# Kernel tuning notes

Measured on AMD Instinct MI355X. Metric: run time of the kernel, lower is better.

The kernel has to match this reference:

```python
import jax, jax.numpy as jnp
import numpy as np
from jax import lax

K = 7            # pool_size / PSROI_BINS
C_OUT = 10       # output channels per bin (features has K*K*C_OUT channels)
FEAT_STRIDE = 16
LAMDA = 0.1
SAMPLES = 2      # bilinear sample points per bin side
H = W = 200
C_IN = K * K * C_OUT  # 490
N_ROIS = 512


def setup_inputs() -> dict:
    key = jax.random.key(0)
    k1, k2, k3, k4 = jax.random.split(key, 4)
    features = jax.random.normal(k1, (1, H, W, C_IN), jnp.float32)
    conv_w = jax.random.truncated_normal(k2, -2.0, 2.0, (3, 3, C_IN, 2 * K * K), jnp.float32) * 0.01
    img = H * FEAT_STRIDE  # image-space extent
    cxy = jax.random.uniform(k3, (N_ROIS, 2), minval=0.0, maxval=img - 1.0)
    wh = jax.random.uniform(k4, (N_ROIS, 2), minval=64.0, maxval=640.0)
    x1 = jnp.clip(cxy[:, 0] - wh[:, 0] * 0.5, 0.0, img - 2.0)
    y1 = jnp.clip(cxy[:, 1] - wh[:, 1] * 0.5, 0.0, img - 2.0)
    x2 = jnp.clip(x1 + wh[:, 0], x1 + 1.0, img - 1.0)
    y2 = jnp.clip(y1 + wh[:, 1], y1 + 1.0, img - 1.0)
    rois = jnp.stack([jnp.zeros(N_ROIS), x1, y1, x2, y2], axis=-1)  # [N,5]
    return {"features": features, "rois": rois, "conv_w": conv_w}


def _bilinear(feat, y, x):
    """feat [H,W,C]; y,x arbitrary equal shapes -> [..., C]."""
    Hf, Wf = feat.shape[0], feat.shape[1]
    y = jnp.clip(y, 0.0, Hf - 1.0)
    x = jnp.clip(x, 0.0, Wf - 1.0)
    y0 = jnp.floor(y)
    x0 = jnp.floor(x)
    y0i = y0.astype(jnp.int32)
    x0i = x0.astype(jnp.int32)
    y1i = jnp.minimum(y0i + 1, Hf - 1)
    x1i = jnp.minimum(x0i + 1, Wf - 1)
    wy = (y - y0)[..., None]
    wx = (x - x0)[..., None]
    v00 = feat[y0i, x0i]
    v01 = feat[y0i, x1i]
    v10 = feat[y1i, x0i]
    v11 = feat[y1i, x1i]
    return (v00 * (1 - wy) * (1 - wx) + v01 * (1 - wy) * wx
            + v10 * wy * (1 - wx) + v11 * wy * wx)


def _ps_roi(feat, box, cpg, offsets):
    """Position-sensitive RoI avg pooling with optional per-bin offsets.
    feat [H,W,K*K*cpg]; box (x1,y1,x2,y2) image coords; offsets [K,K,2] (dx,dy)
    in image coords or None. Returns [K,K,cpg]."""
    x1, y1, x2, y2 = box
    fx1 = x1 / FEAT_STRIDE
    fy1 = y1 / FEAT_STRIDE
    bw = (x2 - x1 + 1.0) / FEAT_STRIDE / K
    bh = (y2 - y1 + 1.0) / FEAT_STRIDE / K
    idx = jnp.arange(K, dtype=feat.dtype)
    s = (jnp.arange(SAMPLES, dtype=feat.dtype) + 0.5) / SAMPLES
    sx = fx1 + (idx[:, None] + s[None, :]) * bw  # [K(j), S]
    sy = fy1 + (idx[:, None] + s[None, :]) * bh  # [K(i), S]
    gx = jnp.broadcast_to(sx[None, :, None, :], (K, K, SAMPLES, SAMPLES))
    gy = jnp.broadcast_to(sy[:, None, :, None], (K, K, SAMPLES, SAMPLES))
    if offsets is not None:
        off = offsets / FEAT_STRIDE  # image -> feature coords
        gx = gx + off[..., 0][:, :, None, None]
        gy = gy + off[..., 1][:, :, None, None]
    vals = _bilinear(feat, gy, gx)                     # [K,K,S,S,K*K*cpg]
    vals = vals.reshape(K, K, SAMPLES, SAMPLES, K * K, cpg)
    bin_idx = (jnp.arange(K)[:, None] * K + jnp.arange(K)[None, :])  # [K,K]
    sel = jnp.take_along_axis(
        vals, bin_idx[:, :, None, None, None, None], axis=4)[..., 0, :]
    return sel.mean(axis=(2, 3))  # [K,K,cpg]


def reference(features, rois, conv_w):
    # 3x3 same conv producing 2*K*K offset channels (no bias)
    offset_map = lax.conv_general_dilated(
        features, conv_w, (1, 1), 'SAME',
        dimension_numbers=('NHWC', 'HWIO', 'NHWC'))[0]  # [H,W,2*K*K]
    feat0 = features[0]  # [H,W,K*K*C_OUT]

    def one_roi(roi):
        x1, y1, x2, y2 = roi[1], roi[2], roi[3], roi[4]
        rw = x2 - x1 + 1.0
        rh = y2 - y1 + 1.0
        box = (x1, y1, x2, y2)
        # stage 1: pool the offset map position-sensitively -> [K,K,2]
        off = _ps_roi(offset_map, box, 2, None).reshape(-1, 2)
        off = jnp.stack((off[:, 0] * rw * LAMDA,
                         off[:, 1] * rh * LAMDA), axis=-1).reshape(K, K, 2)
        # stage 2: deformable PS-RoI pooling of the features -> [K,K,C_OUT]
        return _ps_roi(feat0, box, C_OUT, off)

    return jax.vmap(one_roi)(rois)  # [N, K, K, C_OUT]
```

## Files before the change

### kernel.cpp

```cpp
#include <hip/hip_runtime.h>
#include <hip/hip_bf16.h>

#define Hh   200
#define Ww   200
#define CIN  490
#define OCN  98
#define KK   7
#define COUT 10
#define NROIS 512
#define PIX  8

#define PH   202
#define PW   202
#define PC   512
#define NPIX (Hh * Ww)
#define KCN  16
#define NF   7
#define NUNITS 144
#define NGRAN  36

typedef __attribute__((ext_vector_type(8))) short short8;
typedef __attribute__((ext_vector_type(4))) float float4v;

__global__ __launch_bounds__(256) void pack_feat_kernel(
    const float* __restrict__ feat, __hip_bfloat16* __restrict__ pf)
{
    int tid = blockIdx.x * 256 + threadIdx.x;
    if (tid >= PH * PW * (PC / 8)) return;
    int c8  = (tid & 63) * 8;
    int pix = tid >> 6;
    int py = pix / PW, px = pix % PW;
    __hip_bfloat16* dst = pf + (size_t)pix * PC + c8;
    bool interior = (py >= 1 && py <= Hh && px >= 1 && px <= Ww);

    __hip_bfloat16 v[8];
    if (interior && c8 + 8 <= CIN) {
        const float* s = feat + ((size_t)(py - 1) * Ww + (px - 1)) * CIN + c8;
#pragma unroll
        for (int q = 0; q < 4; ++q) {
            float2 f2 = *reinterpret_cast<const float2*>(s + q * 2);
            v[q * 2]     = __float2bfloat16(f2.x);
            v[q * 2 + 1] = __float2bfloat16(f2.y);
        }
    } else {
        const float* s = interior ? feat + ((size_t)(py - 1) * Ww + (px - 1)) * CIN : nullptr;
#pragma unroll
        for (int j = 0; j < 8; ++j) {
            float val = (interior && (c8 + j) < CIN) ? s[c8 + j] : 0.f;
            v[j] = __float2bfloat16(val);
        }
    }
    *reinterpret_cast<short8*>(dst) = *reinterpret_cast<short8*>(v);
}

__global__ __launch_bounds__(256) void pack_w_kernel(
    const float* __restrict__ w, __hip_bfloat16* __restrict__ bp)
{
    int idx = blockIdx.x * 256 + threadIdx.x;
    if (idx >= NUNITS * NF * 64 * 8) return;
    int j = idx & 7;
    int l = (idx >> 3) & 63;
    int f = (idx >> 9) % NF;
    int u = idx / (NF * 512);
    int tap = u / KCN, kc = u % KCN;
    int k = kc * 32 + ((l >> 4) * 8) + j;
    int n = f * 16 + (l & 15);
    float val = (k < CIN && n < OCN) ? w[((size_t)tap * CIN + k) * OCN + n] : 0.f;
    bp[idx] = __float2bfloat16(val);
}

__global__ __launch_bounds__(640) void conv_mfma_kernel(
    const short* __restrict__ pf,
    const short* __restrict__ bp,
    float* __restrict__ om)
{
    __shared__ short bsm[8 * 3584];

    int l = threadIdx.x & 63;
    int w = threadIdx.x >> 6;
    int m0 = blockIdx.x * 160 + w * 16;

    int row = m0 + (l & 15);
    int y = row / Ww, x = row % Ww;
    const short* abase = pf + ((size_t)(y * PW + x) * PC) + ((l >> 4) * 8);

    float4v acc[NF];
#pragma unroll
    for (int f = 0; f < NF; ++f) acc[f] = (float4v){0.f, 0.f, 0.f, 0.f};

    auto aAddr = [&](int u) -> const short* {
        int tap = u >> 4, kc = u & 15;
        int ky = tap / 3, kx = tap % 3;
        return abase + (ky * PW + kx) * PC + kc * 32;
    };

    {
#pragma unroll
        for (int s = 0; s < 3; ++s) {
            int i = w + s * 10;
            if (i < 28) {
                int u = i / 7, f = i % 7;
                short8 v = *reinterpret_cast<const short8*>(
                    bp + ((size_t)(u * NF + f)) * 512 + l * 8);
                *reinterpret_cast<short8*>(&bsm[(u & 7) * 3584 + f * 512 + l * 8]) = v;
            }
        }
    }
    short8 a0 = *reinterpret_cast<const short8*>(aAddr(0));
    short8 a1 = *reinterpret_cast<const short8*>(aAddr(1));
    short8 a2 = *reinterpret_cast<const short8*>(aAddr(2));
    short8 a3 = *reinterpret_cast<const short8*>(aAddr(3));
    __syncthreads();

    for (int g = 0; g < NGRAN; ++g) {
        bool more = (g < NGRAN - 1);
        int u0n = (g + 1) * 4;

        short8 st0, st1, st2;
        int off0 = -1, off1 = -1, off2 = -1;
        if (more) {
            {
                int i = w;
                int uu = u0n + i / 7, f = i % 7;
                st0 = *reinterpret_cast<const short8*>(
                    bp + ((size_t)(uu * NF + f)) * 512 + l * 8);
                off0 = (uu & 7) * 3584 + f * 512 + l * 8;
            }
            {
                int i = w + 10;
                int uu = u0n + i / 7, f = i % 7;
                st1 = *reinterpret_cast<const short8*>(
                    bp + ((size_t)(uu * NF + f)) * 512 + l * 8);
                off1 = (uu & 7) * 3584 + f * 512 + l * 8;
            }
            if (w + 20 < 28) {
                int i = w + 20;
                int uu = u0n + i / 7, f = i % 7;
                st2 = *reinterpret_cast<const short8*>(
                    bp + ((size_t)(uu * NF + f)) * 512 + l * 8);
                off2 = (uu & 7) * 3584 + f * 512 + l * 8;
            }
        }
        short8 n0, n1, n2, n3;
        if (more) {
            n0 = *reinterpret_cast<const short8*>(aAddr(u0n + 0));
            n1 = *reinterpret_cast<const short8*>(aAddr(u0n + 1));
            n2 = *reinterpret_cast<const short8*>(aAddr(u0n + 2));
            n3 = *reinterpret_cast<const short8*>(aAddr(u0n + 3));
        }

        int u0 = g * 4;
#define COMPUTE_UNIT(J, AREG)                                                   \
        {                                                                       \
            int sbase = ((u0 + J) & 7) * 3584 + l * 8;                          \
            _Pragma("unroll")                                                   \
            for (int f = 0; f < NF; ++f) {                                      \
                short8 b = *reinterpret_cast<short8*>(&bsm[sbase + f * 512]);   \
                acc[f] = __builtin_amdgcn_mfma_f32_16x16x32_bf16(               \
                    AREG, b, acc[f], 0, 0, 0);                                  \
            }                                                                   \
        }
        COMPUTE_UNIT(0, a0)
        COMPUTE_UNIT(1, a1)
        COMPUTE_UNIT(2, a2)
        COMPUTE_UNIT(3, a3)
#undef COMPUTE_UNIT

        if (off0 >= 0) *reinterpret_cast<short8*>(&bsm[off0]) = st0;
        if (off1 >= 0) *reinterpret_cast<short8*>(&bsm[off1]) = st1;
        if (off2 >= 0) *reinterpret_cast<short8*>(&bsm[off2]) = st2;
        if (more) { a0 = n0; a1 = n1; a2 = n2; a3 = n3; }
        __syncthreads();
    }

    int n = l & 15;
    int rbase = m0 + ((l >> 4) * 4);
#pragma unroll
    for (int f = 0; f < NF; ++f) {
        int col = f * 16 + n;
        if (col < OCN) {
#pragma unroll
            for (int j = 0; j < 4; ++j)
                om[(size_t)(rbase + j) * OCN + col] = acc[f][j];
        }
    }
}

__global__ __launch_bounds__(256) void conv3x3_kernel(
    const float* __restrict__ feat, const float* __restrict__ w,
    const float* __restrict__ zero, float* __restrict__ om)
{
    int idx = blockIdx.x * blockDim.x + threadIdx.x;
    if (idx >= Hh * (Ww / PIX) * OCN) return;
    int oc = idx % OCN;
    int g  = idx / OCN;
    int x0 = (g % (Ww / PIX)) * PIX;
    int y  = g / (Ww / PIX);

    float acc[PIX];
#pragma unroll
    for (int p = 0; p < PIX; ++p) acc[p] = 0.f;

    for (int ky = 0; ky < 3; ++ky) {
        int yy = y + ky - 1;
        if (yy < 0 || yy >= Hh) continue;
        const float* frow = feat + (size_t)yy * Ww * CIN;
        for (int kx = 0; kx < 3; ++kx) {
            const float* wp = w + ((ky * 3 + kx) * CIN) * OCN + oc;
            const float* fp[PIX];
#pragma unroll
            for (int p = 0; p < PIX; ++p) {
                int xx = x0 + p + kx - 1;
                fp[p] = (xx >= 0 && xx < Ww) ? (frow + (size_t)xx * CIN) : zero;
            }
            for (int ic = 0; ic < CIN; ic += 2) {
                float w0 = wp[ic * OCN];
                float w1 = wp[(ic + 1) * OCN];
#pragma unroll
                for (int p = 0; p < PIX; ++p) {
                    float2 f = *reinterpret_cast<const float2*>(fp[p] + ic);
                    acc[p] = fmaf(f.x, w0, acc[p]);
                    acc[p] = fmaf(f.y, w1, acc[p]);
                }
            }
        }
    }
    float* orow = om + ((size_t)y * Ww + x0) * OCN + oc;
#pragma unroll
    for (int p = 0; p < PIX; ++p) orow[p * OCN] = acc[p];
}

__device__ __forceinline__ void bilin_setup(float y, float x,
    int& i00, int& i01, int& i10, int& i11,
    float& w00, float& w01, float& w10, float& w11)
{
    y = fminf(fmaxf(y, 0.f), 199.f);
    x = fminf(fmaxf(x, 0.f), 199.f);
    float y0f = floorf(y), x0f = floorf(x);
    int y0 = (int)y0f, x0i = (int)x0f;
    int y1 = min(y0 + 1, 199), x1 = min(x0i + 1, 199);
    float wy = y - y0f, wx = x - x0f;
    i00 = y0 * Ww + x0i;  i01 = y0 * Ww + x1;
    i10 = y1 * Ww + x0i;  i11 = y1 * Ww + x1;
    w00 = (1.f - wy) * (1.f - wx);
    w01 = (1.f - wy) * wx;
    w10 = wy * (1.f - wx);
    w11 = wy * wx;
}

__global__ __launch_bounds__(256) void psroi_kernel(
    const float* __restrict__ feat, const float* __restrict__ rois,
    const float* __restrict__ om, float* __restrict__ out)
{
    int n = blockIdx.x;
    int t = threadIdx.x;

    float x1 = rois[n * 5 + 1], y1 = rois[n * 5 + 2];
    float x2 = rois[n * 5 + 3], y2 = rois[n * 5 + 4];
    float rw = x2 - x1 + 1.0f, rh = y2 - y1 + 1.0f;
    float fx1 = x1 * 0.0625f, fy1 = y1 * 0.0625f;
    float bw = (rw * 0.0625f) / 7.0f;
    float bh = (rh * 0.0625f) / 7.0f;

    __shared__ float offs[49][2];

    if (t < 49) {
        int bi = t / 7, bj = t % 7;
        float ax = 0.f, ay = 0.f;
#pragma unroll
        for (int ss = 0; ss < 4; ++ss) {
            float sj = ((float)(ss & 1) + 0.5f) * 0.5f;
            float si = ((float)(ss >> 1) + 0.5f) * 0.5f;
            float gx = fx1 + ((float)bj + sj) * bw;
            float gy = fy1 + ((float)bi + si) * bh;
            int i00, i01, i10, i11; float w00, w01, w10, w11;
            bilin_setup(gy, gx, i00, i01, i10, i11, w00, w01, w10, w11);
            int c0 = t * 2;
            const float* p00 = om + (size_t)i00 * OCN + c0;
            const float* p01 = om + (size_t)i01 * OCN + c0;
            const float* p10 = om + (size_t)i10 * OCN + c0;
            const float* p11 = om + (size_t)i11 * OCN + c0;
            ax += w00 * p00[0] + w01 * p01[0] + w10 * p10[0] + w11 * p11[0];
            ay += w00 * p00[1] + w01 * p01[1] + w10 * p10[1] + w11 * p11[1];
        }
        offs[t][0] = ax * 0.25f * rw * 0.1f * 0.0625f;
        offs[t][1] = ay * 0.25f * rh * 0.1f * 0.0625f;
    }
    __syncthreads();

    for (int o = t; o < KK * KK * COUT; o += blockDim.x) {
        int bin = o / COUT, c = o % COUT;
        int bi = bin / 7, bj = bin % 7;
        float dx = offs[bin][0], dy = offs[bin][1];
        int ch = bin * COUT + c;
        float acc = 0.f;
#pragma unroll
        for (int ss = 0; ss < 4; ++ss) {
            float sj = ((float)(ss & 1) + 0.5f) * 0.5f;
            float si = ((float)(ss >> 1) + 0.5f) * 0.5f;
            float gx = fx1 + ((float)bj + sj) * bw + dx;
            float gy = fy1 + ((float)bi + si) * bh + dy;
            int i00, i01, i10, i11; float w00, w01, w10, w11;
            bilin_setup(gy, gx, i00, i01, i10, i11, w00, w01, w10, w11);
            acc += w00 * feat[(size_t)i00 * CIN + ch]
                 + w01 * feat[(size_t)i01 * CIN + ch]
                 + w10 * feat[(size_t)i10 * CIN + ch]
                 + w11 * feat[(size_t)i11 * CIN + ch];
        }
        out[(size_t)n * (KK * KK * COUT) + o] = acc * 0.25f;
    }
}

extern "C" void kernel_launch(void* const* d_in, const int* in_sizes, int n_in,
                              void* d_out, int out_size, void* d_ws, size_t ws_size,
                              hipStream_t stream) {
    const float* feat = (const float*)d_in[0];
    const float* rois = (const float*)d_in[1];
    const float* w    = (const float*)d_in[2];
    float* out = (float*)d_out;

    const size_t OM_BYTES = (size_t)NPIX * OCN * 4;
    const size_t BP_BYTES = (size_t)NUNITS * NF * 64 * 8 * 2;
    const size_t PF_BYTES = (size_t)PH * PW * PC * 2;
    const size_t NEEDED = OM_BYTES + BP_BYTES + PF_BYTES;

    if (ws_size >= NEEDED) {
        float* om = (float*)d_ws;
        __hip_bfloat16* bp = (__hip_bfloat16*)((char*)d_ws + OM_BYTES);
        __hip_bfloat16* pf = (__hip_bfloat16*)((char*)d_ws + OM_BYTES + BP_BYTES);

        int wThreads = NUNITS * NF * 64 * 8;
        pack_w_kernel<<<(wThreads + 255) / 256, 256, 0, stream>>>(w, bp);
        int fThreads = PH * PW * (PC / 8);
        pack_feat_kernel<<<(fThreads + 255) / 256, 256, 0, stream>>>(feat, pf);
        conv_mfma_kernel<<<250, 640, 0, stream>>>(
            (const short*)pf, (const short*)bp, om);
        psroi_kernel<<<NROIS, 256, 0, stream>>>(feat, rois, om, out);
    } else {
        float* zero = (float*)d_ws;
        float* om   = (float*)d_ws + 1024;
        hipMemsetAsync(d_ws, 0, 4096, stream);
        int convThreads = Hh * (Ww / PIX) * OCN;
        conv3x3_kernel<<<(convThreads + 255) / 256, 256, 0, stream>>>(feat, w, zero, om);
        psroi_kernel<<<NROIS, 256, 0, stream>>>(feat, rois, om, out);
    }
}
```

Before: 96.75 us.

## Register-block two M tiles per wave and remap blocks for XCD locality

Each wave now computes two 16-row M tiles sharing every B fragment read from LDS, with blocks of 5 waves instead of 10, so each LDS B load feeds two MFMAs. Block indices are also remapped so consecutive M tiles land on the same XCD, aiming to improve L2 reuse of the overlapping 3x3 input rows. The cost is more accumulator and A-fragment registers per wave, fewer waves per block for latency hiding, and more staging loads per wave.

```diff
diff --git a/kernel.cpp b/kernel.cpp
--- a/kernel.cpp
+++ b/kernel.cpp
@@ -18,6 +18,9 @@
 #define NF   7
 #define NUNITS 144
 #define NGRAN  36
+#define MR   2
+#define NWAVES 5
+#define BLK_M (NWAVES * MR * 16)
 
 typedef __attribute__((ext_vector_type(8))) short short8;
 typedef __attribute__((ext_vector_type(4))) float float4v;
@@ -69,119 +72,147 @@
     bp[idx] = __float2bfloat16(val);
 }
 
-__global__ __launch_bounds__(640) void conv_mfma_kernel(
+__global__ __launch_bounds__(320) void conv_mfma_kernel(
     const short* __restrict__ pf,
     const short* __restrict__ bp,
     float* __restrict__ om)
 {
     __shared__ short bsm[8 * 3584];
 
+    int orig = blockIdx.x;
+    int xcd = orig & 7;
+    int pos = orig >> 3;
+    int blk = ((xcd < 2) ? xcd * 32 : 64 + (xcd - 2) * 31) + pos;
+
     int l = threadIdx.x & 63;
     int w = threadIdx.x >> 6;
-    int m0 = blockIdx.x * 160 + w * 16;
-
-    int row = m0 + (l & 15);
-    int y = row / Ww, x = row % Ww;
-    const short* abase = pf + ((size_t)(y * PW + x) * PC) + ((l >> 4) * 8);
-
-    float4v acc[NF];
-#pragma unroll
-    for (int f = 0; f < NF; ++f) acc[f] = (float4v){0.f, 0.f, 0.f, 0.f};
-
-    auto aAddr = [&](int u) -> const short* {
+    int m0 = blk * BLK_M + w * (MR * 16);
+
+    const short* abase0;
+    const short* abase1;
+    {
+        int row0 = m0 + (l & 15);
+        int row1 = m0 + 16 + (l & 15);
+        int y0 = row0 / Ww, x0 = row0 % Ww;
+        int y1 = row1 / Ww, x1 = row1 % Ww;
+        abase0 = pf + ((size_t)(y0 * PW + x0) * PC) + ((l >> 4) * 8);
+        abase1 = pf + ((size_t)(y1 * PW + x1) * PC) + ((l >> 4) * 8);
+    }
+    const short* bbase = bp + l * 8;
+
+    float4v acc[MR][NF];
+#pragma unroll
+    for (int r = 0; r < MR; ++r)
+#pragma unroll
+        for (int f = 0; f < NF; ++f) acc[r][f] = (float4v){0.f, 0.f, 0.f, 0.f};
+
+    auto aOff = [&](int u) -> int {
         int tap = u >> 4, kc = u & 15;
         int ky = tap / 3, kx = tap % 3;
-        return abase + (ky * PW + kx) * PC + kc * 32;
+        return (ky * PW + kx) * PC + kc * 32;
     };
 
-    {
-#pragma unroll
-        for (int s = 0; s < 3; ++s) {
-            int i = w + s * 10;
-            if (i < 28) {
-                int u = i / 7, f = i % 7;
-                short8 v = *reinterpret_cast<const short8*>(
-                    bp + ((size_t)(u * NF + f)) * 512 + l * 8);
-                *reinterpret_cast<short8*>(&bsm[(u & 7) * 3584 + f * 512 + l * 8]) = v;
-            }
-        }
-    }
-    short8 a0 = *reinterpret_cast<const short8*>(aAddr(0));
-    short8 a1 = *reinterpret_cast<const short8*>(aAddr(1));
-    short8 a2 = *reinterpret_cast<const short8*>(aAddr(2));
-    short8 a3 = *reinterpret_cast<const short8*>(aAddr(3));
+#pragma unroll
+    for (int s = 0; s < 6; ++s) {
+        int i = w + s * NWAVES;
+        if (i < 28) {
+            int u = i / 7, f = i % 7;
+            short8 v = *reinterpret_cast<const short8*>(
+                bp + ((size_t)(u * NF + f)) * 512 + l * 8);
+            *reinterpret_cast<short8*>(&bsm[(u & 7) * 3584 + f * 512 + l * 8]) = v;
+        }
+    }
+    short8 a00 = *reinterpret_cast<const short8*>(abase0 + aOff(0));
+    short8 a01 = *reinterpret_cast<const short8*>(abase0 + aOff(1));
+    short8 a02 = *reinterpret_cast<const short8*>(abase0 + aOff(2));
+    short8 a03 = *reinterpret_cast<const short8*>(abase0 + aOff(3));
+    short8 a10 = *reinterpret_cast<const short8*>(abase1 + aOff(0));
+    short8 a11 = *reinterpret_cast<const short8*>(abase1 + aOff(1));
+    short8 a12 = *reinterpret_cast<const short8*>(abase1 + aOff(2));
+    short8 a13 = *reinterpret_cast<const short8*>(abase1 + aOff(3));
     __syncthreads();
 
     for (int g = 0; g < NGRAN; ++g) {
         bool more = (g < NGRAN - 1);
         int u0n = (g + 1) * 4;
 
-        short8 st0, st1, st2;
-        int off0 = -1, off1 = -1, off2 = -1;
+        short8 st0, st1, st2, st3, st4, st5;
+        int off0 = -1, off1 = -1, off2 = -1, off3 = -1, off4 = -1, off5 = -1;
         if (more) {
-            {
-                int i = w;
-                int uu = u0n + i / 7, f = i % 7;
-                st0 = *reinterpret_cast<const short8*>(
-                    bp + ((size_t)(uu * NF + f)) * 512 + l * 8);
-                off0 = (uu & 7) * 3584 + f * 512 + l * 8;
+#define STAGE_LOAD(S, STV, OFFV)                                               \
+            {                                                                  \
+                int i = w + (S) * NWAVES;                                      \
+                if (i < 28) {                                                  \
+                    int uu = u0n + i / 7, f = i % 7;                           \
+                    STV = *reinterpret_cast<const short8*>(                    \
+                        bp + ((size_t)(uu * NF + f)) * 512 + l * 8);           \
+                    OFFV = (uu & 7) * 3584 + f * 512 + l * 8;                  \
+                }                                                              \
             }
-            {
-                int i = w + 10;
-                int uu = u0n + i / 7, f = i % 7;
-                st1 = *reinterpret_cast<const short8*>(
-                    bp + ((size_t)(uu * NF + f)) * 512 + l * 8);
-                off1 = (uu & 7) * 3584 + f * 512 + l * 8;
-            }
-            if (w + 20 < 28) {
-                int i = w + 20;
-                int uu = u0n + i / 7, f = i % 7;
-                st2 = *reinterpret_cast<const short8*>(
-                    bp + ((size_t)(uu * NF + f)) * 512 + l * 8);
-                off2 = (uu & 7) * 3584 + f * 512 + l * 8;
-            }
-        }
-        short8 n0, n1, n2, n3;
+            STAGE_LOAD(0, st0, off0)
+            STAGE_LOAD(1, st1, off1)
+            STAGE_LOAD(2, st2, off2)
+            STAGE_LOAD(3, st3, off3)
+            STAGE_LOAD(4, st4, off4)
+            STAGE_LOAD(5, st5, off5)
+#undef STAGE_LOAD
+        }
+        short8 n00, n01, n02, n03, n10, n11, n12, n13;
         if (more) {
-            n0 = *reinterpret_cast<const short8*>(aAddr(u0n + 0));
-            n1 = *reinterpret_cast<const short8*>(aAddr(u0n + 1));
-            n2 = *reinterpret_cast<const short8*>(aAddr(u0n + 2));
-            n3 = *reinterpret_cast<const short8*>(aAddr(u0n + 3));
+            n00 = *reinterpret_cast<const short8*>(abase0 + aOff(u0n + 0));
+            n01 = *reinterpret_cast<const short8*>(abase0 + aOff(u0n + 1));
+            n02 = *reinterpret_cast<const short8*>(abase0 + aOff(u0n + 2));
+            n03 = *reinterpret_cast<const short8*>(abase0 + aOff(u0n + 3));
+            n10 = *reinterpret_cast<const short8*>(abase1 + aOff(u0n + 0));
+            n11 = *reinterpret_cast<const short8*>(abase1 + aOff(u0n + 1));
+            n12 = *reinterpret_cast<const short8*>(abase1 + aOff(u0n + 2));
+            n13 = *reinterpret_cast<const short8*>(abase1 + aOff(u0n + 3));
         }
 
         int u0 = g * 4;
-#define COMPUTE_UNIT(J, AREG)                                                   \
+#define COMPUTE_UNIT(J, AR0, AR1)                                               \
         {                                                                       \
             int sbase = ((u0 + J) & 7) * 3584 + l * 8;                          \
             _Pragma("unroll")                                                   \
             for (int f = 0; f < NF; ++f) {                                      \
                 short8 b = *reinterpret_cast<short8*>(&bsm[sbase + f * 512]);   \
-                acc[f] = __builtin_amdgcn_mfma_f32_16x16x32_bf16(               \
-                    AREG, b, acc[f], 0, 0, 0);                                  \
+                acc[0][f] = __builtin_amdgcn_mfma_f32_16x16x32_bf16(            \
+                    AR0, b, acc[0][f], 0, 0, 0);                                \
+                acc[1][f] = __builtin_amdgcn_mfma_f32_16x16x32_bf16(            \
+                    AR1, b, acc[1][f], 0, 0, 0);                                \
             }                                                                   \
         }
-        COMPUTE_UNIT(0, a0)
-        COMPUTE_UNIT(1, a1)
-        COMPUTE_UNIT(2, a2)
-        COMPUTE_UNIT(3, a3)
+        COMPUTE_UNIT(0, a00, a10)
+        COMPUTE_UNIT(1, a01, a11)
+        COMPUTE_UNIT(2, a02, a12)
+        COMPUTE_UNIT(3, a03, a13)
 #undef COMPUTE_UNIT
 
         if (off0 >= 0) *reinterpret_cast<short8*>(&bsm[off0]) = st0;
         if (off1 >= 0) *reinterpret_cast<short8*>(&bsm[off1]) = st1;
         if (off2 >= 0) *reinterpret_cast<short8*>(&bsm[off2]) = st2;
-        if (more) { a0 = n0; a1 = n1; a2 = n2; a3 = n3; }
+        if (off3 >= 0) *reinterpret_cast<short8*>(&bsm[off3]) = st3;
+        if (off4 >= 0) *reinterpret_cast<short8*>(&bsm[off4]) = st4;
+        if (off5 >= 0) *reinterpret_cast<short8*>(&bsm[off5]) = st5;
+        if (more) {
+            a00 = n00; a01 = n01; a02 = n02; a03 = n03;
+            a10 = n10; a11 = n11; a12 = n12; a13 = n13;
+        }
         __syncthreads();
     }
 
     int n = l & 15;
-    int rbase = m0 + ((l >> 4) * 4);
-#pragma unroll
-    for (int f = 0; f < NF; ++f) {
-        int col = f * 16 + n;
-        if (col < OCN) {
-#pragma unroll
-            for (int j = 0; j < 4; ++j)
-                om[(size_t)(rbase + j) * OCN + col] = acc[f][j];
+#pragma unroll
+    for (int r = 0; r < MR; ++r) {
+        int rbase = m0 + r * 16 + ((l >> 4) * 4);
+#pragma unroll
+        for (int f = 0; f < NF; ++f) {
+            int col = f * 16 + n;
+            if (col < OCN) {
+#pragma unroll
+                for (int j = 0; j < 4; ++j)
+                    om[(size_t)(rbase + j) * OCN + col] = acc[r][f][j];
+            }
         }
     }
 }
@@ -333,7 +364,7 @@
         pack_w_kernel<<<(wThreads + 255) / 256, 256, 0, stream>>>(w, bp);
         int fThreads = PH * PW * (PC / 8);
         pack_feat_kernel<<<(fThreads + 255) / 256, 256, 0, stream>>>(feat, pf);
-        conv_mfma_kernel<<<250, 640, 0, stream>>>(
+        conv_mfma_kernel<<<250, 320, 0, stream>>>(
             (const short*)pf, (const short*)bp, om);
         psroi_kernel<<<NROIS, 256, 0, stream>>>(feat, rois, om, out);
     } else {
```

New measurement: 106.0 us. +9.5%, slower.

## Split conv MFMA tile per wave into 32 rows by half the N columns

Applied to the files above, without the earlier changes.

Each wave in the conv MFMA kernel now covers 32 output rows and roughly half of the N tiles (4 or 3 of 7), where before it covered 16 rows and all 7 N tiles. Each B fragment read from LDS now feeds two MFMAs, which cuts LDS traffic per MFMA. The cost is twice the A-fragment global loads per wave (the same A rows are loaded by both waves of a pair) and more A registers. The nh split is also uneven, 4 versus 3 tiles, so the two waves in a pair do unequal work.

```diff
diff --git a/kernel.cpp b/kernel.cpp
--- a/kernel.cpp
+++ b/kernel.cpp
@@ -18,6 +18,7 @@
 #define NF   7
 #define NUNITS 144
 #define NGRAN  36
+#define BLK_M 160
 
 typedef __attribute__((ext_vector_type(8))) short short8;
 typedef __attribute__((ext_vector_type(4))) float float4v;
@@ -78,38 +79,51 @@
 
     int l = threadIdx.x & 63;
     int w = threadIdx.x >> 6;
-    int m0 = blockIdx.x * 160 + w * 16;
-
-    int row = m0 + (l & 15);
-    int y = row / Ww, x = row % Ww;
-    const short* abase = pf + ((size_t)(y * PW + x) * PC) + ((l >> 4) * 8);
-
-    float4v acc[NF];
-#pragma unroll
-    for (int f = 0; f < NF; ++f) acc[f] = (float4v){0.f, 0.f, 0.f, 0.f};
-
-    auto aAddr = [&](int u) -> const short* {
+    int mpos = w >> 1;
+    int nh = w & 1;
+    int m0 = blockIdx.x * BLK_M + mpos * 32;
+
+    const short* abase0;
+    const short* abase1;
+    {
+        int row0 = m0 + (l & 15);
+        int row1 = m0 + 16 + (l & 15);
+        int y0 = row0 / Ww, x0 = row0 % Ww;
+        int y1 = row1 / Ww, x1 = row1 % Ww;
+        abase0 = pf + ((size_t)(y0 * PW + x0) * PC) + ((l >> 4) * 8);
+        abase1 = pf + ((size_t)(y1 * PW + x1) * PC) + ((l >> 4) * 8);
+    }
+
+    float4v acc[2][4];
+#pragma unroll
+    for (int r = 0; r < 2; ++r)
+#pragma unroll
+        for (int f = 0; f < 4; ++f) acc[r][f] = (float4v){0.f, 0.f, 0.f, 0.f};
+
+    auto aOff = [&](int u) -> int {
         int tap = u >> 4, kc = u & 15;
         int ky = tap / 3, kx = tap % 3;
-        return abase + (ky * PW + kx) * PC + kc * 32;
+        return (ky * PW + kx) * PC + kc * 32;
     };
 
-    {
-#pragma unroll
-        for (int s = 0; s < 3; ++s) {
-            int i = w + s * 10;
-            if (i < 28) {
-                int u = i / 7, f = i % 7;
-                short8 v = *reinterpret_cast<const short8*>(
-                    bp + ((size_t)(u * NF + f)) * 512 + l * 8);
-                *reinterpret_cast<short8*>(&bsm[(u & 7) * 3584 + f * 512 + l * 8]) = v;
-            }
-        }
-    }
-    short8 a0 = *reinterpret_cast<const short8*>(aAddr(0));
-    short8 a1 = *reinterpret_cast<const short8*>(aAddr(1));
-    short8 a2 = *reinterpret_cast<const short8*>(aAddr(2));
-    short8 a3 = *reinterpret_cast<const short8*>(aAddr(3));
+#pragma unroll
+    for (int s = 0; s < 3; ++s) {
+        int i = w + s * 10;
+        if (i < 28) {
+            int u = i / 7, f = i % 7;
+            short8 v = *reinterpret_cast<const short8*>(
+                bp + ((size_t)(u * NF + f)) * 512 + l * 8);
+            *reinterpret_cast<short8*>(&bsm[(u & 7) * 3584 + f * 512 + l * 8]) = v;
+        }
+    }
+    short8 a00 = *reinterpret_cast<const short8*>(abase0 + aOff(0));
+    short8 a01 = *reinterpret_cast<const short8*>(abase0 + aOff(1));
+    short8 a02 = *reinterpret_cast<const short8*>(abase0 + aOff(2));
+    short8 a03 = *reinterpret_cast<const short8*>(abase0 + aOff(3));
+    short8 a10 = *reinterpret_cast<const short8*>(abase1 + aOff(0));
+    short8 a11 = *reinterpret_cast<const short8*>(abase1 + aOff(1));
+    short8 a12 = *reinterpret_cast<const short8*>(abase1 + aOff(2));
+    short8 a13 = *reinterpret_cast<const short8*>(abase1 + aOff(3));
     __syncthreads();
 
     for (int g = 0; g < NGRAN; ++g) {
@@ -141,47 +155,67 @@
                 off2 = (uu & 7) * 3584 + f * 512 + l * 8;
             }
         }
-        short8 n0, n1, n2, n3;
+        short8 n00, n01, n02, n03, n10, n11, n12, n13;
         if (more) {
-            n0 = *reinterpret_cast<const short8*>(aAddr(u0n + 0));
-            n1 = *reinterpret_cast<const short8*>(aAddr(u0n + 1));
-            n2 = *reinterpret_cast<const short8*>(aAddr(u0n + 2));
-            n3 = *reinterpret_cast<const short8*>(aAddr(u0n + 3));
+            n00 = *reinterpret_cast<const short8*>(abase0 + aOff(u0n + 0));
+            n01 = *reinterpret_cast<const short8*>(abase0 + aOff(u0n + 1));
+            n02 = *reinterpret_cast<const short8*>(abase0 + aOff(u0n + 2));
+            n03 = *reinterpret_cast<const short8*>(abase0 + aOff(u0n + 3));
+            n10 = *reinterpret_cast<const short8*>(abase1 + aOff(u0n + 0));
+            n11 = *reinterpret_cast<const short8*>(abase1 + aOff(u0n + 1));
+            n12 = *reinterpret_cast<const short8*>(abase1 + aOff(u0n + 2));
+            n13 = *reinterpret_cast<const short8*>(abase1 + aOff(u0n + 3));
         }
 
         int u0 = g * 4;
-#define COMPUTE_UNIT(J, AREG)                                                   \
+#define COMPUTE_UNIT(J, AR0, AR1, F0, F1, FBASE)                                \
         {                                                                       \
             int sbase = ((u0 + J) & 7) * 3584 + l * 8;                          \
             _Pragma("unroll")                                                   \
-            for (int f = 0; f < NF; ++f) {                                      \
+            for (int f = F0; f < F1; ++f) {                                     \
                 short8 b = *reinterpret_cast<short8*>(&bsm[sbase + f * 512]);   \
-                acc[f] = __builtin_amdgcn_mfma_f32_16x16x32_bf16(               \
-                    AREG, b, acc[f], 0, 0, 0);                                  \
+                acc[0][f - FBASE] = __builtin_amdgcn_mfma_f32_16x16x32_bf16(    \
+                    AR0, b, acc[0][f - FBASE], 0, 0, 0);                        \
+                acc[1][f - FBASE] = __builtin_amdgcn_mfma_f32_16x16x32_bf16(    \
+                    AR1, b, acc[1][f - FBASE], 0, 0, 0);                        \
             }                                                                   \
         }
-        COMPUTE_UNIT(0, a0)
-        COMPUTE_UNIT(1, a1)
-        COMPUTE_UNIT(2, a2)
-        COMPUTE_UNIT(3, a3)
+        if (nh == 0) {
+            COMPUTE_UNIT(0, a00, a10, 0, 4, 0)
+            COMPUTE_UNIT(1, a01, a11, 0, 4, 0)
+            COMPUTE_UNIT(2, a02, a12, 0, 4, 0)
+            COMPUTE_UNIT(3, a03, a13, 0, 4, 0)
+        } else {
+            COMPUTE_UNIT(0, a00, a10, 4, 7, 4)
+            COMPUTE_UNIT(1, a01, a11, 4, 7, 4)
+            COMPUTE_UNIT(2, a02, a12, 4, 7, 4)
+            COMPUTE_UNIT(3, a03, a13, 4, 7, 4)
+        }
 #undef COMPUTE_UNIT
 
         if (off0 >= 0) *reinterpret_cast<short8*>(&bsm[off0]) = st0;
         if (off1 >= 0) *reinterpret_cast<short8*>(&bsm[off1]) = st1;
         if (off2 >= 0) *reinterpret_cast<short8*>(&bsm[off2]) = st2;
-        if (more) { a0 = n0; a1 = n1; a2 = n2; a3 = n3; }
+        if (more) {
+            a00 = n00; a01 = n01; a02 = n02; a03 = n03;
+            a10 = n10; a11 = n11; a12 = n12; a13 = n13;
+        }
         __syncthreads();
     }
 
     int n = l & 15;
-    int rbase = m0 + ((l >> 4) * 4);
-#pragma unroll
-    for (int f = 0; f < NF; ++f) {
-        int col = f * 16 + n;
-        if (col < OCN) {
-#pragma unroll
-            for (int j = 0; j < 4; ++j)
-                om[(size_t)(rbase + j) * OCN + col] = acc[f][j];
+    int fbeg = nh ? 4 : 0;
+    int fend = nh ? 7 : 4;
+#pragma unroll
+    for (int r = 0; r < 2; ++r) {
+        int rbase = m0 + r * 16 + ((l >> 4) * 4);
+        for (int f = fbeg; f < fend; ++f) {
+            int col = f * 16 + n;
+            if (col < OCN) {
+#pragma unroll
+                for (int j = 0; j < 4; ++j)
+                    om[(size_t)(rbase + j) * OCN + col] = acc[r][f - fbeg][j];
+            }
         }
     }
 }
```

Measured after the change: 133.0 us. +37.5%, slower.

## Reorder conv K-loop to tap-inner and remap blocks contiguously per XCD

Applied to the files above, without the earlier changes.

The packed weight layout and the A-operand address order now iterate the 9 conv taps inside each 32-channel chunk rather than all 16 chunks inside each tap. Block indices are also remapped so each XCD processes a contiguous range of output rows. Both aim to improve L2 locality of the padded feature reads, since neighbouring taps hit overlapping cache lines and spatially adjacent blocks share one XCD's L2. The remap hard-codes 250 blocks split as 32,32 then 31 per XCD, and the address math now needs divide-by-9 in place of shifts.

```diff
diff --git a/kernel.cpp b/kernel.cpp
--- a/kernel.cpp
+++ b/kernel.cpp
@@ -62,7 +62,7 @@
     int l = (idx >> 3) & 63;
     int f = (idx >> 9) % NF;
     int u = idx / (NF * 512);
-    int tap = u / KCN, kc = u % KCN;
+    int kc = u / 9, tap = u % 9;
     int k = kc * 32 + ((l >> 4) * 8) + j;
     int n = f * 16 + (l & 15);
     float val = (k < CIN && n < OCN) ? w[((size_t)tap * CIN + k) * OCN + n] : 0.f;
@@ -76,9 +76,14 @@
 {
     __shared__ short bsm[8 * 3584];
 
+    int orig = blockIdx.x;
+    int xcd = orig & 7;
+    int pos = orig >> 3;
+    int blk = ((xcd < 2) ? xcd * 32 : 64 + (xcd - 2) * 31) + pos;
+
     int l = threadIdx.x & 63;
     int w = threadIdx.x >> 6;
-    int m0 = blockIdx.x * 160 + w * 16;
+    int m0 = blk * 160 + w * 16;
 
     int row = m0 + (l & 15);
     int y = row / Ww, x = row % Ww;
@@ -88,28 +93,26 @@
 #pragma unroll
     for (int f = 0; f < NF; ++f) acc[f] = (float4v){0.f, 0.f, 0.f, 0.f};
 
-    auto aAddr = [&](int u) -> const short* {
-        int tap = u >> 4, kc = u & 15;
-        int ky = tap / 3, kx = tap % 3;
-        return abase + (ky * PW + kx) * PC + kc * 32;
+    auto aOff = [&](int u) -> int {
+        int kc = u / 9, tap = u - kc * 9;
+        int ky = tap / 3, kx = tap - ky * 3;
+        return (ky * PW + kx) * PC + kc * 32;
     };
 
-    {
-#pragma unroll
-        for (int s = 0; s < 3; ++s) {
-            int i = w + s * 10;
-            if (i < 28) {
-                int u = i / 7, f = i % 7;
-                short8 v = *reinterpret_cast<const short8*>(
-                    bp + ((size_t)(u * NF + f)) * 512 + l * 8);
-                *reinterpret_cast<short8*>(&bsm[(u & 7) * 3584 + f * 512 + l * 8]) = v;
-            }
-        }
-    }
-    short8 a0 = *reinterpret_cast<const short8*>(aAddr(0));
-    short8 a1 = *reinterpret_cast<const short8*>(aAddr(1));
-    short8 a2 = *reinterpret_cast<const short8*>(aAddr(2));
-    short8 a3 = *reinterpret_cast<const short8*>(aAddr(3));
+#pragma unroll
+    for (int s = 0; s < 3; ++s) {
+        int i = w + s * 10;
+        if (i < 28) {
+            int u = i / 7, f = i % 7;
+            short8 v = *reinterpret_cast<const short8*>(
+                bp + ((size_t)(u * NF + f)) * 512 + l * 8);
+            *reinterpret_cast<short8*>(&bsm[(u & 7) * 3584 + f * 512 + l * 8]) = v;
+        }
+    }
+    short8 a0 = *reinterpret_cast<const short8*>(abase + aOff(0));
+    short8 a1 = *reinterpret_cast<const short8*>(abase + aOff(1));
+    short8 a2 = *reinterpret_cast<const short8*>(abase + aOff(2));
+    short8 a3 = *reinterpret_cast<const short8*>(abase + aOff(3));
     __syncthreads();
 
     for (int g = 0; g < NGRAN; ++g) {
@@ -143,10 +146,10 @@
         }
         short8 n0, n1, n2, n3;
         if (more) {
-            n0 = *reinterpret_cast<const short8*>(aAddr(u0n + 0));
-            n1 = *reinterpret_cast<const short8*>(aAddr(u0n + 1));
-            n2 = *reinterpret_cast<const short8*>(aAddr(u0n + 2));
-            n3 = *reinterpret_cast<const short8*>(aAddr(u0n + 3));
+            n0 = *reinterpret_cast<const short8*>(abase + aOff(u0n + 0));
+            n1 = *reinterpret_cast<const short8*>(abase + aOff(u0n + 1));
+            n2 = *reinterpret_cast<const short8*>(abase + aOff(u0n + 2));
+            n3 = *reinterpret_cast<const short8*>(abase + aOff(u0n + 3));
         }
 
         int u0 = g * 4;
```

After: 93.19 us. 3.7% less time.
